# Kernel tuning notes

Measured on AMD Instinct MI355X. Metric: run time of the kernel, lower is better.

Reference implementation:

```python
import jax, jax.numpy as jnp
import numpy as np

TEMPERATURE = 0.05


def setup_inputs() -> dict:
    key = jax.random.key(0)
    k1, k2, k3 = jax.random.split(key, 3)
    B, D = 8192, 256
    return {
        "embedding_anchor": jax.random.normal(k1, (B, D), dtype=jnp.float32),
        "embedding_pos": jax.random.normal(k2, (B, D), dtype=jnp.float32),
        "embedding_neg": jax.random.normal(k3, (B, D), dtype=jnp.float32),
    }


def _l2norm(x, eps=1e-12):
    # torch.nn.functional.normalize: x / max(||x||, eps)
    n = jnp.sqrt(jnp.sum(x * x, axis=1, keepdims=True))
    return x / jnp.maximum(n, eps)


def reference(embedding_anchor, embedding_pos, embedding_neg):
    B = embedding_anchor.shape[0]
    targets = jnp.concatenate([embedding_pos, embedding_neg], axis=0)  # [2B, D]
    a = _l2norm(embedding_anchor)
    t = _l2norm(targets)
    scores = (a @ t.T) / TEMPERATURE  # [B, 2B]
    # Chunked CE with per-chunk weight len(labels)/B == full-batch mean CE
    logp = jax.nn.log_softmax(scores, axis=1)
    labels = jnp.arange(B)
    loss = -jnp.mean(jnp.take_along_axis(logp, labels[:, None], axis=1))
    return loss
```

## Files before the change

kernel.cpp:

```cpp
#include <hip/hip_runtime.h>
#include <hip/hip_bf16.h>

#define D 256
#define TEMP_INV 20.0f
#define K_EXP2 28.85390081777927f
#define NJ 16
#define NS (NJ * 4)

typedef __attribute__((ext_vector_type(8))) short bf16x8s;
typedef __attribute__((ext_vector_type(4))) float f32x4;

__device__ __forceinline__ unsigned short f2bf(float f) {
  unsigned u = __float_as_uint(f);
  unsigned r = u + 0x7FFFu + ((u >> 16) & 1u);
  return (unsigned short)(r >> 16);
}

__device__ __forceinline__ void gld16(const void* g, void* l) {
  __builtin_amdgcn_global_load_lds(
      (const __attribute__((address_space(1))) void*)g,
      (__attribute__((address_space(3))) void*)l, 16, 0, 0);
}

__global__ __launch_bounds__(256) void nce_normalize(const float* __restrict__ anc,
                                                     const float* __restrict__ pos,
                                                     const float* __restrict__ neg,
                                                     unsigned short* __restrict__ An,
                                                     unsigned short* __restrict__ Tn,
                                                     float* __restrict__ rowsum,
                                                     int B) {
  int zi = blockIdx.x * 256 + threadIdx.x;
  if (blockIdx.x < (B + 255) / 256 && zi < B) rowsum[zi] = 0.0f;

  const int lane = threadIdx.x & 63;
  const int wid  = threadIdx.x >> 6;
  const int sub  = lane >> 4, lr = lane & 15;
  int row = blockIdx.x * 16 + wid * 4 + sub;

  const float* src;
  unsigned short* dst;
  int r2;
  if (row < B)          { src = anc; dst = An; r2 = row; }
  else if (row < 2 * B) { src = pos; dst = Tn; r2 = row - B; }
  else                  { src = neg; dst = Tn + (size_t)B * D; r2 = row - 2 * B; }

  const float4* sp = reinterpret_cast<const float4*>(src) + (size_t)r2 * (D / 4);
  float4 v[4];
#pragma unroll
  for (int c = 0; c < 4; ++c) v[c] = sp[lr + c * 16];
  float ss = 0.0f;
#pragma unroll
  for (int c = 0; c < 4; ++c)
    ss += v[c].x * v[c].x + v[c].y * v[c].y + v[c].z * v[c].z + v[c].w * v[c].w;
  ss += __shfl_xor(ss, 1, 64);
  ss += __shfl_xor(ss, 2, 64);
  ss += __shfl_xor(ss, 4, 64);
  ss += __shfl_xor(ss, 8, 64);
  float inv = rsqrtf(fmaxf(ss, 1e-24f));
  ushort4* dp = reinterpret_cast<ushort4*>(dst) + (size_t)r2 * (D / 4);
#pragma unroll
  for (int c = 0; c < 4; ++c) {
    ushort4 o;
    o.x = f2bf(v[c].x * inv);
    o.y = f2bf(v[c].y * inv);
    o.z = f2bf(v[c].z * inv);
    o.w = f2bf(v[c].w * inv);
    dp[lr + c * 16] = o;
  }
}

__global__ __launch_bounds__(256, 2) void nce_scores(const unsigned short* __restrict__ A,
                                                     const unsigned short* __restrict__ T,
                                                     float* __restrict__ rowsum,
                                                     float* __restrict__ diag) {
  __shared__ unsigned char smem[4][16384];

  const int tid  = threadIdx.x;
  const int lane = tid & 63;
  const int wid  = __builtin_amdgcn_readfirstlane(tid >> 6);
  const int wr = wid >> 1, wc = wid & 1;
  const int row0 = blockIdx.y * 128;
  const int cg   = blockIdx.x;
  const int r = lane & 15, g = lane >> 4;

  const int Rl = lane >> 3;
  const int Cl = (lane & 7) ^ Rl;
  const unsigned char* gB = (const unsigned char*)T +
      (((size_t)(cg * 2048 + wid * 32 + Rl)) << 9) + Cl * 16;

  auto STAGE = [&](int s) {
    const unsigned char* gb = gB + (size_t)(s >> 2) * 65536 + (s & 3) * 128;
    unsigned char* sb = &smem[s & 3][0];
#pragma unroll
    for (int q = 0; q < 4; ++q)
      gld16(gb + q * 4096, sb + wid * 4096 + q * 1024);
  };

  const int rx = r & 7;
  int offB[2][4];
#pragma unroll
  for (int ks = 0; ks < 2; ++ks)
#pragma unroll
    for (int n = 0; n < 4; ++n)
      offB[ks][n] = wc * 8192 + n * 2048 + r * 128 + ((((ks << 2) | g) ^ rx) << 4);

  const unsigned short* aPtr = A + (size_t)(row0 + wr * 64 + r) * D + g * 8;
  bf16x8s aF[4][8];
#pragma unroll
  for (int m = 0; m < 4; ++m)
#pragma unroll
    for (int t = 0; t < 8; ++t)
      aF[m][t] = *reinterpret_cast<const bf16x8s*>(aPtr + (size_t)m * 16 * D + t * 32);
  __builtin_amdgcn_sched_barrier(0);

  STAGE(0);
  STAGE(1);
  STAGE(2);

  float rs[4][4];
#pragma unroll
  for (int m = 0; m < 4; ++m)
#pragma unroll
    for (int reg = 0; reg < 4; ++reg) rs[m][reg] = 0.0f;

  for (int j = 0; j < NJ; ++j) {
    f32x4 acc[4][4];
#pragma unroll
    for (int m = 0; m < 4; ++m)
#pragma unroll
      for (int n = 0; n < 4; ++n) acc[m][n] = (f32x4)0.0f;

#pragma unroll
    for (int kt = 0; kt < 4; ++kt) {
      const int s = j * 4 + kt;
      asm volatile("s_waitcnt vmcnt(8)" ::: "memory");
      __builtin_amdgcn_s_barrier();
      const unsigned char* sb = &smem[kt][0];
      bf16x8s bF[2][4];
#pragma unroll
      for (int ks = 0; ks < 2; ++ks)
#pragma unroll
        for (int n = 0; n < 4; ++n)
          bF[ks][n] = *reinterpret_cast<const bf16x8s*>(sb + offB[ks][n]);
      if (s + 3 < NS) STAGE(s + 3);
      asm volatile("s_waitcnt lgkmcnt(0)" ::: "memory");
      __builtin_amdgcn_sched_barrier(0);
      __builtin_amdgcn_s_setprio(1);
#pragma unroll
      for (int ks = 0; ks < 2; ++ks)
#pragma unroll
        for (int m = 0; m < 4; ++m)
#pragma unroll
          for (int n = 0; n < 4; ++n)
            acc[m][n] = __builtin_amdgcn_mfma_f32_16x16x32_bf16(
                aF[m][kt * 2 + ks], bF[ks][n], acc[m][n], 0, 0, 0);
      __builtin_amdgcn_s_setprio(0);
      __builtin_amdgcn_sched_barrier(0);
    }

    const bool diagTile = (cg * NJ + j == (int)blockIdx.y);
#pragma unroll
    for (int m = 0; m < 4; ++m) {
#pragma unroll
      for (int reg = 0; reg < 4; ++reg) {
        float s = 0.0f;
#pragma unroll
        for (int n = 0; n < 4; ++n)
          s += __builtin_amdgcn_exp2f(acc[m][n][reg] * K_EXP2);
        rs[m][reg] += s;
        if (diagTile && wr == wc && r == g * 4 + reg)
          diag[row0 + wr * 64 + m * 16 + r] = acc[m][m][reg];
      }
    }
  }

#pragma unroll
  for (int m = 0; m < 4; ++m) {
#pragma unroll
    for (int reg = 0; reg < 4; ++reg) {
      float s = rs[m][reg];
      s += __shfl_xor(s, 1, 64);
      s += __shfl_xor(s, 2, 64);
      s += __shfl_xor(s, 4, 64);
      s += __shfl_xor(s, 8, 64);
      if (r == 0) atomicAdd(&rowsum[row0 + wr * 64 + m * 16 + g * 4 + reg], s);
    }
  }
}

__global__ __launch_bounds__(1024) void nce_finalize(const float* __restrict__ rowsum,
                                                     const float* __restrict__ diag,
                                                     float* __restrict__ out, int n) {
  __shared__ float red[16];
  float s = 0.0f;
  for (int i = threadIdx.x; i < n; i += 1024)
    s += logf(rowsum[i]) - diag[i] * TEMP_INV;
#pragma unroll
  for (int m = 1; m < 64; m <<= 1) s += __shfl_xor(s, m, 64);
  if ((threadIdx.x & 63) == 0) red[threadIdx.x >> 6] = s;
  __syncthreads();
  if (threadIdx.x == 0) {
    float t = 0.0f;
#pragma unroll
    for (int i = 0; i < 16; ++i) t += red[i];
    out[0] = t / (float)n;
  }
}

extern "C" void kernel_launch(void* const* d_in, const int* in_sizes, int n_in,
                              void* d_out, int out_size, void* d_ws, size_t ws_size,
                              hipStream_t stream) {
  const float* anc = (const float*)d_in[0];
  const float* pos = (const float*)d_in[1];
  const float* neg = (const float*)d_in[2];
  const int B  = in_sizes[0] / D;
  const int N2 = 2 * B;

  char* ws = (char*)d_ws;
  unsigned short* An = (unsigned short*)ws;
  unsigned short* Tn = (unsigned short*)(ws + (size_t)B * D * 2);
  float* rowsum = (float*)(ws + (size_t)B * D * 2 + (size_t)N2 * D * 2);
  float* diag   = rowsum + B;

  nce_normalize<<<3 * B / 16, 256, 0, stream>>>(anc, pos, neg, An, Tn, rowsum, B);

  dim3 grid(N2 / (NJ * 128), B / 128);
  nce_scores<<<grid, 256, 0, stream>>>(An, Tn, rowsum, diag);

  nce_finalize<<<1, 1024, 0, stream>>>(rowsum, diag, (float*)d_out, B);
}
```

Before: 139.2 us.

## Load B operand fragments directly from global into registers, dropping LDS staging

Replaces the four-stage LDS ring (global_load_lds, barriers, swizzled LDS reads) with per-wave direct global loads of B fragments into a double-buffered register set. Each new load is issued right after the MFMAs that consumed the same register buffer. This removes LDS traffic and block-wide barriers. In exchange, each wave fetches its own B columns, so the two waves sharing columns load them twice from L2. The global load latency is also hidden by only one k-step of MFMAs.

Measured after the change: 219.9 us. 58.0% more time.

```diff
diff --git a/kernel.cpp b/kernel.cpp
--- a/kernel.cpp
+++ b/kernel.cpp
@@ -5,7 +5,6 @@
 #define TEMP_INV 20.0f
 #define K_EXP2 28.85390081777927f
 #define NJ 16
-#define NS (NJ * 4)
 
 typedef __attribute__((ext_vector_type(8))) short bf16x8s;
 typedef __attribute__((ext_vector_type(4))) float f32x4;
@@ -14,12 +13,6 @@
   unsigned u = __float_as_uint(f);
   unsigned r = u + 0x7FFFu + ((u >> 16) & 1u);
   return (unsigned short)(r >> 16);
-}
-
-__device__ __forceinline__ void gld16(const void* g, void* l) {
-  __builtin_amdgcn_global_load_lds(
-      (const __attribute__((address_space(1))) void*)g,
-      (__attribute__((address_space(3))) void*)l, 16, 0, 0);
 }
 
 __global__ __launch_bounds__(256) void nce_normalize(const float* __restrict__ anc,
@@ -73,8 +66,6 @@
                                                      const unsigned short* __restrict__ T,
                                                      float* __restrict__ rowsum,
                                                      float* __restrict__ diag) {
-  __shared__ unsigned char smem[4][16384];
-
   const int tid  = threadIdx.x;
   const int lane = tid & 63;
   const int wid  = __builtin_amdgcn_readfirstlane(tid >> 6);
@@ -83,26 +74,11 @@
   const int cg   = blockIdx.x;
   const int r = lane & 15, g = lane >> 4;
 
-  const int Rl = lane >> 3;
-  const int Cl = (lane & 7) ^ Rl;
-  const unsigned char* gB = (const unsigned char*)T +
-      (((size_t)(cg * 2048 + wid * 32 + Rl)) << 9) + Cl * 16;
-
-  auto STAGE = [&](int s) {
-    const unsigned char* gb = gB + (size_t)(s >> 2) * 65536 + (s & 3) * 128;
-    unsigned char* sb = &smem[s & 3][0];
-#pragma unroll
-    for (int q = 0; q < 4; ++q)
-      gld16(gb + q * 4096, sb + wid * 4096 + q * 1024);
-  };
-
-  const int rx = r & 7;
-  int offB[2][4];
-#pragma unroll
-  for (int ks = 0; ks < 2; ++ks)
-#pragma unroll
-    for (int n = 0; n < 4; ++n)
-      offB[ks][n] = wc * 8192 + n * 2048 + r * 128 + ((((ks << 2) | g) ^ rx) << 4);
+  const unsigned char* bPtr[4];
+#pragma unroll
+  for (int n = 0; n < 4; ++n)
+    bPtr[n] = (const unsigned char*)T +
+              (((size_t)(cg * 2048 + wc * 64 + n * 16 + r)) << 9) + g * 16;
 
   const unsigned short* aPtr = A + (size_t)(row0 + wr * 64 + r) * D + g * 8;
   bf16x8s aF[4][8];
@@ -111,17 +87,20 @@
 #pragma unroll
     for (int t = 0; t < 8; ++t)
       aF[m][t] = *reinterpret_cast<const bf16x8s*>(aPtr + (size_t)m * 16 * D + t * 32);
-  __builtin_amdgcn_sched_barrier(0);
-
-  STAGE(0);
-  STAGE(1);
-  STAGE(2);
 
   float rs[4][4];
 #pragma unroll
   for (int m = 0; m < 4; ++m)
 #pragma unroll
     for (int reg = 0; reg < 4; ++reg) rs[m][reg] = 0.0f;
+
+  bf16x8s bR[2][4];
+#pragma unroll
+  for (int n = 0; n < 4; ++n)
+    bR[0][n] = *reinterpret_cast<const bf16x8s*>(bPtr[n]);
+#pragma unroll
+  for (int n = 0; n < 4; ++n)
+    bR[1][n] = *reinterpret_cast<const bf16x8s*>(bPtr[n] + 64);
 
   for (int j = 0; j < NJ; ++j) {
     f32x4 acc[4][4];
@@ -130,32 +109,22 @@
 #pragma unroll
       for (int n = 0; n < 4; ++n) acc[m][n] = (f32x4)0.0f;
 
-#pragma unroll
-    for (int kt = 0; kt < 4; ++kt) {
-      const int s = j * 4 + kt;
-      asm volatile("s_waitcnt vmcnt(8)" ::: "memory");
-      __builtin_amdgcn_s_barrier();
-      const unsigned char* sb = &smem[kt][0];
-      bf16x8s bF[2][4];
-#pragma unroll
-      for (int ks = 0; ks < 2; ++ks)
+    const bool lastJ = (j == NJ - 1);
+
+#pragma unroll
+    for (int kt = 0; kt < 8; ++kt) {
+#pragma unroll
+      for (int m = 0; m < 4; ++m)
 #pragma unroll
         for (int n = 0; n < 4; ++n)
-          bF[ks][n] = *reinterpret_cast<const bf16x8s*>(sb + offB[ks][n]);
-      if (s + 3 < NS) STAGE(s + 3);
-      asm volatile("s_waitcnt lgkmcnt(0)" ::: "memory");
-      __builtin_amdgcn_sched_barrier(0);
-      __builtin_amdgcn_s_setprio(1);
-#pragma unroll
-      for (int ks = 0; ks < 2; ++ks)
-#pragma unroll
-        for (int m = 0; m < 4; ++m)
-#pragma unroll
-          for (int n = 0; n < 4; ++n)
-            acc[m][n] = __builtin_amdgcn_mfma_f32_16x16x32_bf16(
-                aF[m][kt * 2 + ks], bF[ks][n], acc[m][n], 0, 0, 0);
-      __builtin_amdgcn_s_setprio(0);
-      __builtin_amdgcn_sched_barrier(0);
+          acc[m][n] = __builtin_amdgcn_mfma_f32_16x16x32_bf16(
+              aF[m][kt], bR[kt & 1][n], acc[m][n], 0, 0, 0);
+      if (!lastJ || kt < 6) {
+        const int off = (kt >= 6) ? (65536 + ((kt - 6) << 6)) : ((kt + 2) << 6);
+#pragma unroll
+        for (int n = 0; n < 4; ++n)
+          bR[kt & 1][n] = *reinterpret_cast<const bf16x8s*>(bPtr[n] + off);
+      }
     }
 
     const bool diagTile = (cg * NJ + j == (int)blockIdx.y);
@@ -172,6 +141,9 @@
           diag[row0 + wr * 64 + m * 16 + r] = acc[m][m][reg];
       }
     }
+
+#pragma unroll
+    for (int n = 0; n < 4; ++n) bPtr[n] += 65536;
   }
 
 #pragma unroll
```
